# Kernel optimization log

Measured on AMD Instinct MI355X. Metric: run time of the kernel, lower is better.

## Reference

```python
import jax, jax.numpy as jnp
import numpy as np
from jax import lax

B, C, H, W = 8, 64, 64, 64
C8 = C // 8
EPS = 1e-5


def setup_inputs() -> dict:
    key = jax.random.key(0)
    ks = jax.random.split(key, 10)
    s = lambda *sh: 0.02
    inp = {
        "x": jax.random.normal(ks[0], (B, C, H, W), dtype=jnp.float32),
        "conv_b_w": jax.random.normal(ks[1], (C8, C), dtype=jnp.float32) * 0.05,
        "conv_b_b": jnp.zeros((C8,), jnp.float32),
        "conv_c_w": jax.random.normal(ks[2], (C8, C), dtype=jnp.float32) * 0.05,
        "conv_c_b": jnp.zeros((C8,), jnp.float32),
        "conv_d_w": jax.random.normal(ks[3], (C, C), dtype=jnp.float32) * 0.05,
        "conv_d_b": jnp.zeros((C,), jnp.float32),
        "alpha": jnp.zeros((1,), jnp.float32) + 0.1,  # learned PAM scale
        "beta": jnp.zeros((1,), jnp.float32) + 0.1,   # learned CAM scale
        "conv_w": jax.random.normal(ks[4], (2 * C, C, 3, 3), dtype=jnp.float32) * 0.02,
        "conv_bias": jnp.zeros((2 * C,), jnp.float32),
        "bn_gamma": jnp.ones((2 * C,), jnp.float32),
        "bn_beta": jnp.zeros((2 * C,), jnp.float32),
    }
    return inp


def _conv1x1(x, w, b):
    # x: [B,C,H,W], w: [O,C] -> [B,O,H,W]
    return jnp.einsum('oc,bchw->bohw', w, x) + b[None, :, None, None]


def _forward(x, conv_b_w, conv_b_b, conv_c_w, conv_c_b, conv_d_w, conv_d_b,
             alpha, beta, conv_w, conv_bias, bn_gamma, bn_beta):
    b, c, h, w = x.shape
    n = h * w
    # ---- Position Attention Module ----
    feat_b = _conv1x1(x, conv_b_w, conv_b_b).reshape(b, C8, n)   # [B,C8,N]
    feat_c = _conv1x1(x, conv_c_w, conv_c_b).reshape(b, C8, n)   # [B,C8,N]
    # torch: bmm(feat_b^T [B,N,C8], feat_c [B,C8,N]) -> [B,N,N]
    attn_s = jax.nn.softmax(jnp.einsum('bcn,bcm->bnm', feat_b, feat_c), axis=-1)
    feat_d = _conv1x1(x, conv_d_w, conv_d_b).reshape(b, c, n)    # [B,C,N]
    # torch: bmm(feat_d, attn_s^T) -> out[b,c,n] = sum_m feat_d[b,c,m]*attn[b,n,m]
    feat_e = jnp.einsum('bcm,bnm->bcn', feat_d, attn_s).reshape(b, c, h, w)
    x = alpha[0] * feat_e + x
    # ---- Channel Attention Module ----
    fa = x.reshape(b, c, n)                                      # [B,C,N]
    att = jnp.einsum('bcn,bdn->bcd', fa, fa)                     # [B,C,C]
    att_new = jnp.max(att, axis=-1, keepdims=True) - att
    att = jax.nn.softmax(att_new, axis=-1)
    fe = jnp.einsum('bcd,bdn->bcn', att, fa).reshape(b, c, h, w)
    x = beta[0] * fe + x
    # ---- conv3x3 + BN (batch stats) + ReLU + maxpool(2,2,pad=(1,0)) ----
    out = lax.conv_general_dilated(x, conv_w, (1, 1), ((1, 1), (1, 1)),
                                   dimension_numbers=('NCHW', 'OIHW', 'NCHW'))
    out = out + conv_bias[None, :, None, None]
    mean = jnp.mean(out, axis=(0, 2, 3), keepdims=True)
    var = jnp.var(out, axis=(0, 2, 3), keepdims=True)
    out = (out - mean) * lax.rsqrt(var + EPS)
    out = out * bn_gamma[None, :, None, None] + bn_beta[None, :, None, None]
    out = jax.nn.relu(out)
    # MaxPool2d(kernel=2, stride=2, padding=(1,0)): -inf padding on height only
    out = lax.reduce_window(out, -jnp.inf, lax.max,
                            (1, 1, 2, 2), (1, 1, 2, 2),
                            ((0, 0), (0, 0), (1, 1), (0, 0)))
    return out


def reference(x, conv_b_w, conv_b_b, conv_c_w, conv_c_b, conv_d_w, conv_d_b,
              alpha, beta, conv_w, conv_bias, bn_gamma, bn_beta):
    return _forward(x, conv_b_w, conv_b_b, conv_c_w, conv_c_b, conv_d_w, conv_d_b,
                    alpha, beta, conv_w, conv_bias, bn_gamma, bn_beta)
```

## Files before the change

### kernel.cpp

```cpp
#include <hip/hip_runtime.h>

using f32x4  = __attribute__((ext_vector_type(4))) float;
using f32x16 = __attribute__((ext_vector_type(16))) float;
using bf16x8 = __attribute__((ext_vector_type(8))) short;
using u32x4  = __attribute__((ext_vector_type(4))) unsigned int;
using u32x2  = __attribute__((ext_vector_type(2))) unsigned int;
typedef unsigned short u16;

__device__ __forceinline__ u16 f2bf(float f) {
  unsigned u = __float_as_uint(f);
  unsigned r = (u + 0x7FFFu + ((u >> 16) & 1u)) >> 16;
  return (u16)r;
}

#if __has_builtin(__builtin_amdgcn_exp2f)
#define FAST_EXP2(x) __builtin_amdgcn_exp2f(x)
#else
#define FAST_EXP2(x) __expf(0.6931471805599453f * (x))
#endif

#define LOG2E 1.4426950408889634f

__device__ __forceinline__ void permswap32(unsigned& a, unsigned& b) {
  asm volatile("v_permlane32_swap_b32 %0, %1" : "+v"(a), "+v"(b));
}

__global__ void __launch_bounds__(256) k1_conv1x1(
    const float* __restrict__ x, const float* __restrict__ wB, const float* __restrict__ bB,
    const float* __restrict__ wC, const float* __restrict__ bC,
    const float* __restrict__ wD, const float* __restrict__ bD,
    u16* __restrict__ featBb, u16* __restrict__ featCb, u16* __restrict__ featD,
    const float* __restrict__ cw, u16* __restrict__ wb) {
  const int t = threadIdx.x;
  const int b = blockIdx.y;
  const int z = blockIdx.z;
  if (z == 3) {
    int gid = (b * 16 + blockIdx.x) * 256 + t;
#pragma unroll
    for (int k = 0; k < 3; ++k) {
      int F = gid + k * 32768;
      if (F < 73728) {
        int j = F & 7, lane = (F >> 3) & 63, T = F >> 9;
        int tap = T >> 4, g = (T >> 1) & 7, kc = T & 1;
        int l16 = lane & 15, quad = lane >> 4;
        int oc = g * 16 + l16, ic = kc * 32 + quad * 8 + j;
        wb[F] = f2bf(cw[(oc * 64 + ic) * 9 + tap]);
      }
    }
    return;
  }
  __shared__ float W[2048];
  __shared__ float Bias[32];
  const int n = blockIdx.x * 256 + t;
  if (z == 0) {
    for (int i = t; i < 512; i += 256) W[i] = wB[i];
    for (int i = t; i < 512; i += 256) W[512 + i] = wC[i];
    if (t < 8) Bias[t] = bB[t];
    if (t >= 8 && t < 16) Bias[t] = bC[t - 8];
  } else {
    const float* wsrc = wD + (z - 1) * 2048;
    for (int i = t; i < 2048; i += 256) W[i] = wsrc[i];
    if (t < 32) Bias[t] = bD[(z - 1) * 32 + t];
  }
  __syncthreads();
  float xv[64];
#pragma unroll
  for (int c = 0; c < 64; ++c) xv[c] = x[((b * 64 + c) << 12) + n];
  if (z == 0) {
    float o[16];
#pragma unroll
    for (int k = 0; k < 16; ++k) {
      f32x4 s = {0.f, 0.f, 0.f, 0.f};
#pragma unroll
      for (int cq = 0; cq < 16; ++cq) {
        f32x4 wv = *(const f32x4*)&W[k * 64 + cq * 4];
        f32x4 xq = {xv[cq * 4], xv[cq * 4 + 1], xv[cq * 4 + 2], xv[cq * 4 + 3]};
        s += wv * xq;
      }
      o[k] = Bias[k] + s[0] + s[1] + s[2] + s[3];
    }
    int base = ((b << 12) + n) * 8;
    u32x4 pb, pc;
#pragma unroll
    for (int i = 0; i < 4; ++i) {
      pb[i] = (unsigned)f2bf(o[2 * i] * LOG2E) | ((unsigned)f2bf(o[2 * i + 1] * LOG2E) << 16);
      pc[i] = (unsigned)f2bf(o[8 + 2 * i]) | ((unsigned)f2bf(o[8 + 2 * i + 1]) << 16);
    }
    *(u32x4*)&featBb[base] = pb;
    *(u32x4*)&featCb[base] = pc;
  } else {
#pragma unroll 4
    for (int k = 0; k < 32; ++k) {
      f32x4 s = {0.f, 0.f, 0.f, 0.f};
#pragma unroll
      for (int cq = 0; cq < 16; ++cq) {
        f32x4 wv = *(const f32x4*)&W[k * 64 + cq * 4];
        f32x4 xq = {xv[cq * 4], xv[cq * 4 + 1], xv[cq * 4 + 2], xv[cq * 4 + 3]};
        s += wv * xq;
      }
      float val = Bias[k] + s[0] + s[1] + s[2] + s[3];
      featD[((b * 64 + (z - 1) * 32 + k) << 12) + n] = f2bf(val);
    }
  }
}

__global__ void __launch_bounds__(256) k2_pam_part(
    const u16* __restrict__ fBb, const u16* __restrict__ fCb, const u16* __restrict__ fD,
    u16* __restrict__ numPart, float* __restrict__ denPart) {
  __shared__ u16 Df[64 * 132];
  const int t = threadIdx.x, b = blockIdx.y, z = blockIdx.z;
  const int w = t >> 6, lane = t & 63, l32 = lane & 31, hi = lane >> 5;
  const int nb = blockIdx.x * 128 + w * 32;
  const int mz = z << 10;

  bf16x8 bq = (bf16x8)(short)0;
  if (hi == 0) bq = *(const bf16x8*)&fBb[(((b << 12) + nb + l32) << 3)];

  f32x16 acc[2];
#pragma unroll
  for (int ct = 0; ct < 2; ++ct) acc[ct] = (f32x16)(0.0f);
  float denp = 0.f;

  for (int ch = 0; ch < 8; ++ch) {
    const int m0 = mz + (ch << 7);
    __syncthreads();
#pragma unroll
    for (int hh = 0; hh < 4; ++hh) {
      int idx = hh * 256 + t;
      int r = idx >> 4, mo = (idx & 15) << 3;
      *(u32x4*)&Df[r * 132 + mo] = *(const u32x4*)&fD[((b * 64 + r) << 12) + m0 + mo];
    }
    __syncthreads();
#pragma unroll
    for (int mt2 = 0; mt2 < 4; ++mt2) {
      bf16x8 af = (bf16x8)(short)0;
      if (hi == 0) af = *(const bf16x8*)&fCb[(((b << 12) + m0 + mt2 * 32 + l32) << 3)];

      unsigned u0[8];
      {
        f32x16 s = __builtin_amdgcn_mfma_f32_32x32x16_bf16(af, bq, (f32x16)(0.0f), 0, 0, 0);
        float dsum = 0.f;
#pragma unroll
        for (int i = 0; i < 8; ++i) {
          float e0 = FAST_EXP2(s[2 * i]);
          float e1 = FAST_EXP2(s[2 * i + 1]);
          dsum += e0 + e1;
          u0[i] = __builtin_amdgcn_perm(__float_as_uint(e1), __float_as_uint(e0), 0x07060302u);
        }
        denp += dsum;
      }
      permswap32(u0[0], u0[2]); permswap32(u0[1], u0[3]);
      permswap32(u0[4], u0[6]); permswap32(u0[5], u0[7]);

#pragma unroll
      for (int kc = 0; kc < 2; ++kc) {
        u32x4 q0 = {u0[4 * kc], u0[4 * kc + 1], u0[4 * kc + 2], u0[4 * kc + 3]};
        bf16x8 bv0 = *(bf16x8*)&q0;
#pragma unroll
        for (int ct = 0; ct < 2; ++ct) {
          bf16x8 av = *(const bf16x8*)&Df[(ct * 32 + l32) * 132 + mt2 * 32 + kc * 16 + hi * 8];
          acc[ct] = __builtin_amdgcn_mfma_f32_32x32x16_bf16(av, bv0, acc[ct], 0, 0, 0);
        }
      }
    }
  }

  const int zb = z * 8 + b;
#pragma unroll
  for (int ct = 0; ct < 2; ++ct)
#pragma unroll
    for (int r = 0; r < 16; ++r) {
      int c = ct * 32 + (r & 3) + ((r >> 2) << 3) + (hi << 2);
      numPart[((zb * 64 + c) << 12) + nb + l32] = (u16)(__float_as_uint(acc[ct][r]) >> 16);
    }
  {
    float d = denp + __shfl_xor(denp, 32);
    if (hi == 0) denPart[(zb << 12) + nb + l32] = d;
  }
}

__global__ void __launch_bounds__(256) k3_gram(
    const u16* __restrict__ numPart, const float* __restrict__ denPart,
    const float* __restrict__ x, const float* __restrict__ alpha,
    float* __restrict__ x1, float* __restrict__ attPart) {
  __shared__ float X[64 * 132];
  __shared__ float Dinv[128];
  const int t = threadIdx.x, b = blockIdx.y, cx = blockIdx.x;
  const int n0 = cx * 128;
  if (t < 128) {
    float den = 0.f;
#pragma unroll
    for (int z = 0; z < 4; ++z) den += denPart[(((z * 8 + b) << 12)) + n0 + t];
    Dinv[t] = alpha[0] / den;
  }
  __syncthreads();
  for (int idx = t; idx < 4096; idx += 256) {
    int row = idx >> 6, cp = (idx & 63) * 2;
    int gi = ((b * 64 + row) << 12) + n0 + cp;
    float num0 = 0.f, num1 = 0.f;
#pragma unroll
    for (int z = 0; z < 4; ++z) {
      unsigned v = *(const unsigned*)&numPart[(((z * 8 + b) * 64 + row) << 12) + n0 + cp];
      num0 += __uint_as_float(v << 16);
      num1 += __uint_as_float(v & 0xFFFF0000u);
    }
    float v0 = num0 * Dinv[cp] + x[gi];
    float v1 = num1 * Dinv[cp + 1] + x[gi + 1];
    X[row * 132 + cp] = v0;
    X[row * 132 + cp + 1] = v1;
    x1[gi] = v0;
    x1[gi + 1] = v1;
  }
  __syncthreads();
  const int cg = t >> 4, dg = t & 15;
  f32x4 acc[4][4];
#pragma unroll
  for (int i = 0; i < 4; ++i)
#pragma unroll
    for (int k = 0; k < 4; ++k) acc[i][k] = (f32x4){0.f, 0.f, 0.f, 0.f};
  for (int nq0 = 0; nq0 < 32; ++nq0) {
    int nq = (nq0 + dg) & 31;
    f32x4 a[4], bb[4];
#pragma unroll
    for (int i = 0; i < 4; ++i) a[i] = *(const f32x4*)&X[(cg * 4 + i) * 132 + nq * 4];
#pragma unroll
    for (int k = 0; k < 4; ++k) bb[k] = *(const f32x4*)&X[(dg * 4 + k) * 132 + nq * 4];
#pragma unroll
    for (int i = 0; i < 4; ++i)
#pragma unroll
      for (int k = 0; k < 4; ++k) acc[i][k] += a[i] * bb[k];
  }
#pragma unroll
  for (int i = 0; i < 4; ++i)
#pragma unroll
    for (int k = 0; k < 4; ++k) {
      f32x4 s = acc[i][k];
      attPart[((b * 32 + cx) * 64 + cg * 4 + i) * 64 + dg * 4 + k] = s[0] + s[1] + s[2] + s[3];
    }
}

__global__ void __launch_bounds__(256) k4_softmax(const float* __restrict__ attPart, float* __restrict__ attP) {
  const int b = blockIdx.y, t = threadIdx.x;
  const int c = (blockIdx.x << 2) + (t >> 6), d = t & 63;
  float v = 0.f;
  for (int p = 0; p < 32; ++p) v += attPart[((b * 32 + p) * 64 + c) * 64 + d];
  float mn = v;
#pragma unroll
  for (int off = 1; off < 64; off <<= 1) mn = fminf(mn, __shfl_xor(mn, off));
  float e = __expf(mn - v);
  float sum = e;
#pragma unroll
  for (int off = 1; off < 64; off <<= 1) sum += __shfl_xor(sum, off);
  attP[(b * 64 + c) * 64 + d] = e / sum;
}

__global__ void __launch_bounds__(256) k5_apply(
    const float* __restrict__ attP, const float* __restrict__ x1,
    const float* __restrict__ beta, u16* __restrict__ x2b) {
  __shared__ float A[64 * 68];
  const int t = threadIdx.x, b = blockIdx.y;
  for (int idx = t; idx < 4096; idx += 256) A[(idx >> 6) * 68 + (idx & 63)] = attP[(b << 12) + idx];
  __syncthreads();
  const int n = blockIdx.x * 64 + (t & 63);
  const int cq = t >> 6;
  const float bv = beta[0];
  float acc[16];
#pragma unroll
  for (int i = 0; i < 16; ++i) acc[i] = 0.f;
  const float* xcol = x1 + ((size_t)b << 18) + n;
#pragma unroll 4
  for (int dq = 0; dq < 16; ++dq) {
    float x0 = xcol[(size_t)(dq * 4 + 0) << 12];
    float x1v = xcol[(size_t)(dq * 4 + 1) << 12];
    float x2 = xcol[(size_t)(dq * 4 + 2) << 12];
    float x3 = xcol[(size_t)(dq * 4 + 3) << 12];
#pragma unroll
    for (int i = 0; i < 16; ++i) {
      const float* av = &A[(cq * 16 + i) * 68 + dq * 4];
      acc[i] += av[0] * x0 + av[1] * x1v + av[2] * x2 + av[3] * x3;
    }
  }
  u16* orow = x2b + ((((size_t)(b << 12) + n) << 6) + cq * 16);
  unsigned pk[8];
#pragma unroll
  for (int i = 0; i < 16; i += 2) {
    float v0 = bv * acc[i] + xcol[(size_t)(cq * 16 + i) << 12];
    float v1 = bv * acc[i + 1] + xcol[(size_t)(cq * 16 + i + 1) << 12];
    pk[i >> 1] = (unsigned)f2bf(v0) | ((unsigned)f2bf(v1) << 16);
  }
  *(u32x4*)&orow[0] = *(u32x4*)&pk[0];
  *(u32x4*)&orow[8] = *(u32x4*)&pk[4];
}

__global__ void __launch_bounds__(256) k6_mfma(const u16* __restrict__ x2b, const u16* __restrict__ wb,
                                               float* __restrict__ y) {
  __shared__ u16 Xl[3 * 66 * 72];
  const int t = threadIdx.x, b = blockIdx.y, h = blockIdx.x;
  for (int idx = t; idx < 3 * 66 * 8; idx += 256) {
    int r = idx / 528;
    int rem = idx - r * 528;
    int c = rem >> 3, icq = rem & 7;
    int gy = h - 1 + r, gx = c - 1;
    u32x4 v = {0u, 0u, 0u, 0u};
    if (gy >= 0 && gy < 64 && gx >= 0 && gx < 64)
      v = *(const u32x4*)&x2b[(((size_t)(b << 6 | gy) << 6) + gx) * 64 + icq * 8];
    *(u32x4*)&Xl[(r * 66 + c) * 72 + icq * 8] = v;
  }
  __syncthreads();
  const int w = t >> 6, lane = t & 63, quad = lane >> 4, l16 = lane & 15;
  const int mBase = (w & 1) * 64;
  const int og = (w & 1) * 4;
  const int nBase = (w >> 1) * 32;
  f32x4 acc[4][2];
#pragma unroll
  for (int ot = 0; ot < 4; ++ot)
#pragma unroll
    for (int nt = 0; nt < 2; ++nt) acc[ot][nt] = (f32x4){0.f, 0.f, 0.f, 0.f};
#pragma unroll 3
  for (int tap = 0; tap < 9; ++tap) {
    const int dy = tap / 3, dx = tap - dy * 3;
    bf16x8 af[4][2];
#pragma unroll
    for (int ot = 0; ot < 4; ++ot)
#pragma unroll
      for (int kc = 0; kc < 2; ++kc)
        af[ot][kc] = *(const bf16x8*)&wb[((((tap * 8 + og + ot) * 2 + kc) << 6) + lane) << 3];
#pragma unroll
    for (int nt = 0; nt < 2; ++nt) {
      const int prow = dy * 66 + nBase + nt * 16 + l16 + dx;
#pragma unroll
      for (int kc = 0; kc < 2; ++kc) {
        bf16x8 bv = *(const bf16x8*)&Xl[prow * 72 + kc * 32 + quad * 8];
#pragma unroll
        for (int ot = 0; ot < 4; ++ot)
          acc[ot][nt] = __builtin_amdgcn_mfma_f32_16x16x32_bf16(af[ot][kc], bv, acc[ot][nt], 0, 0, 0);
      }
    }
  }
#pragma unroll
  for (int ot = 0; ot < 4; ++ot)
#pragma unroll
    for (int nt = 0; nt < 2; ++nt)
#pragma unroll
      for (int r = 0; r < 4; ++r) {
        int oc = mBase + ot * 16 + quad * 4 + r;
        int pix = nBase + nt * 16 + l16;
        y[((b * 128 + oc) << 12) + (h << 6) + pix] = acc[ot][nt][r];
      }
}

__global__ void __launch_bounds__(256) k7_part(const float* __restrict__ y, float* __restrict__ pstats) {
  const int ch = blockIdx.x, q = blockIdx.y, t = threadIdx.x;
  float s = 0.f, ss = 0.f;
#pragma unroll
  for (int bb = 0; bb < 2; ++bb) {
    const float* p = y + (((q * 2 + bb) * 128 + ch) << 12);
#pragma unroll
    for (int i = 0; i < 16; ++i) { float v = p[i * 256 + t]; s += v; ss += v * v; }
  }
#pragma unroll
  for (int off = 1; off < 64; off <<= 1) { s += __shfl_xor(s, off); ss += __shfl_xor(ss, off); }
  __shared__ float rs[4], rss[4];
  if ((t & 63) == 0) { rs[t >> 6] = s; rss[t >> 6] = ss; }
  __syncthreads();
  if (t == 0) {
    pstats[ch * 8 + q * 2]     = rs[0] + rs[1] + rs[2] + rs[3];
    pstats[ch * 8 + q * 2 + 1] = rss[0] + rss[1] + rss[2] + rss[3];
  }
}

__global__ void __launch_bounds__(256) k8_pool(const float* __restrict__ y, const float* __restrict__ pstats,
                                               const float* __restrict__ gamma, const float* __restrict__ bbeta,
                                               float* __restrict__ out) {
  const int bc = blockIdx.x;
  const int ch = bc & 127;
  float S = 0.f, SS = 0.f;
#pragma unroll
  for (int q = 0; q < 4; ++q) { S += pstats[ch * 8 + q * 2]; SS += pstats[ch * 8 + q * 2 + 1]; }
  const float mean = S * (1.f / 32768.f);
  const float var = SS * (1.f / 32768.f) - mean * mean;
  const float sc = gamma[ch] * rsqrtf(var + 1e-5f);
  const float sh = bbeta[ch] - mean * sc;
  const float* p = y + (bc << 12);
  float* op = out + bc * (33 * 32);
  for (int i = threadIdx.x; i < 33 * 32; i += 256) {
    int oh = i >> 5, ow = i & 31;
    int r0 = 2 * oh - 1, r1 = 2 * oh;
    float m = 0.f;
    if (r0 >= 0) {
      m = fmaxf(m, p[r0 * 64 + 2 * ow] * sc + sh);
      m = fmaxf(m, p[r0 * 64 + 2 * ow + 1] * sc + sh);
    }
    if (r1 <= 63) {
      m = fmaxf(m, p[r1 * 64 + 2 * ow] * sc + sh);
      m = fmaxf(m, p[r1 * 64 + 2 * ow + 1] * sc + sh);
    }
    op[i] = m;
  }
}

extern "C" void kernel_launch(void* const* d_in, const int* in_sizes, int n_in,
                              void* d_out, int out_size, void* d_ws, size_t ws_size,
                              hipStream_t stream) {
  const float* x      = (const float*)d_in[0];
  const float* wB     = (const float*)d_in[1];
  const float* bB     = (const float*)d_in[2];
  const float* wC     = (const float*)d_in[3];
  const float* bC     = (const float*)d_in[4];
  const float* wD     = (const float*)d_in[5];
  const float* bD     = (const float*)d_in[6];
  const float* alpha  = (const float*)d_in[7];
  const float* beta   = (const float*)d_in[8];
  const float* cw     = (const float*)d_in[9];
  const float* gamma  = (const float*)d_in[11];
  const float* bnbeta = (const float*)d_in[12];

  char* ws = (char*)d_ws;
  u16*   featBb  = (u16*)  (ws + 0);
  u16*   featCb  = (u16*)  (ws + 524288);
  u16*   fDb     = (u16*)  (ws + 1048576);
  u16*   x2b     = (u16*)  (ws + 0);
  float* x1      = (float*)(ws + 5242880);
  u16*   numPart = (u16*)  (ws + 13631488);
  float* y       = (float*)(ws + 13631488);
  float* denPart = (float*)(ws + 30408704);
  float* attPart = (float*)(ws + 30932992);
  float* attP    = (float*)(ws + 35127296);
  u16*   wb      = (u16*)  (ws + 35258368);
  float* pstats  = (float*)(ws + 35405824);
  float* outp    = (float*)d_out;

  k1_conv1x1<<<dim3(16, 8, 4), 256, 0, stream>>>(x, wB, bB, wC, bC, wD, bD, featBb, featCb, fDb, cw, wb);
  k2_pam_part<<<dim3(32, 8, 4), 256, 0, stream>>>(featBb, featCb, fDb, numPart, denPart);
  k3_gram<<<dim3(32, 8), 256, 0, stream>>>(numPart, denPart, x, alpha, x1, attPart);
  k4_softmax<<<dim3(16, 8), 256, 0, stream>>>(attPart, attP);
  k5_apply<<<dim3(64, 8), 256, 0, stream>>>(attP, x1, beta, x2b);
  k6_mfma<<<dim3(64, 8), 256, 0, stream>>>(x2b, wb, y);
  k7_part<<<dim3(128, 4), 256, 0, stream>>>(y, pstats);
  k8_pool<<<dim3(1024), 256, 0, stream>>>(y, pstats, gamma, bnbeta, outp);
}
```

Measured before the change: 190.9 us.

## Double-buffer PAM value tiles and compute softmax denominator with MFMA

The k2_pam_part kernel now prefetches the next 128-column chunk of feat_d into registers while the current chunk is processed. It stores that chunk into a second LDS buffer, so each iteration needs one barrier instead of two. The four fCb query fragments are loaded up front, ahead of the MFMAs. The softmax denominator is now a third MFMA against a ones-row A operand instead of VALU adds and a cross-lane shuffle. This adds an MFMA per step and more LDS and registers, in exchange for less VALU work and less exposed global-load latency.

```diff
diff --git a/kernel.cpp b/kernel.cpp
--- a/kernel.cpp
+++ b/kernel.cpp
@@ -107,47 +107,66 @@
 __global__ void __launch_bounds__(256) k2_pam_part(
     const u16* __restrict__ fBb, const u16* __restrict__ fCb, const u16* __restrict__ fD,
     u16* __restrict__ numPart, float* __restrict__ denPart) {
-  __shared__ u16 Df[64 * 132];
+  __shared__ u16 Df[2][64 * 132];
   const int t = threadIdx.x, b = blockIdx.y, z = blockIdx.z;
   const int w = t >> 6, lane = t & 63, l32 = lane & 31, hi = lane >> 5;
   const int nb = blockIdx.x * 128 + w * 32;
   const int mz = z << 10;
 
+  int srow[4], smo[4];
+#pragma unroll
+  for (int hh = 0; hh < 4; ++hh) {
+    int idx = hh * 256 + t;
+    srow[hh] = idx >> 4;
+    smo[hh] = (idx & 15) << 3;
+  }
+
   bf16x8 bq = (bf16x8)(short)0;
   if (hi == 0) bq = *(const bf16x8*)&fBb[(((b << 12) + nb + l32) << 3)];
 
-  f32x16 acc[2];
-#pragma unroll
-  for (int ct = 0; ct < 2; ++ct) acc[ct] = (f32x16)(0.0f);
-  float denp = 0.f;
-
+  bf16x8 onesA = (bf16x8)(short)0;
+  if (l32 == 0) onesA = (bf16x8)(short)0x3F80;
+
+  f32x16 acc0 = (f32x16)(0.0f), acc1 = (f32x16)(0.0f), accd = (f32x16)(0.0f);
+
+  u32x4 sreg[4];
+#define K2_ISSUE(CH) {                                                        \
+    int m0_ = mz + ((CH) << 7);                                               \
+    _Pragma("unroll")                                                         \
+    for (int hh = 0; hh < 4; ++hh)                                            \
+      sreg[hh] = *(const u32x4*)&fD[((b * 64 + srow[hh]) << 12) + m0_ + smo[hh]]; }
+#define K2_WRITE(BUF) {                                                       \
+    _Pragma("unroll")                                                         \
+    for (int hh = 0; hh < 4; ++hh)                                            \
+      *(u32x4*)&Df[BUF][srow[hh] * 132 + smo[hh]] = sreg[hh]; }
+
+  K2_ISSUE(0);
+  K2_WRITE(0);
+  __syncthreads();
+
+#pragma unroll 2
   for (int ch = 0; ch < 8; ++ch) {
+    const int cur = ch & 1;
     const int m0 = mz + (ch << 7);
-    __syncthreads();
-#pragma unroll
-    for (int hh = 0; hh < 4; ++hh) {
-      int idx = hh * 256 + t;
-      int r = idx >> 4, mo = (idx & 15) << 3;
-      *(u32x4*)&Df[r * 132 + mo] = *(const u32x4*)&fD[((b * 64 + r) << 12) + m0 + mo];
-    }
-    __syncthreads();
+    if (ch < 7) K2_ISSUE(ch + 1);
+
+    bf16x8 afv[4];
 #pragma unroll
     for (int mt2 = 0; mt2 < 4; ++mt2) {
-      bf16x8 af = (bf16x8)(short)0;
-      if (hi == 0) af = *(const bf16x8*)&fCb[(((b << 12) + m0 + mt2 * 32 + l32) << 3)];
-
+      bf16x8 a = (bf16x8)(short)0;
+      if (hi == 0) a = *(const bf16x8*)&fCb[(((b << 12) + m0 + mt2 * 32 + l32) << 3)];
+      afv[mt2] = a;
+    }
+
+#pragma unroll
+    for (int mt2 = 0; mt2 < 4; ++mt2) {
+      f32x16 s = __builtin_amdgcn_mfma_f32_32x32x16_bf16(afv[mt2], bq, (f32x16)(0.0f), 0, 0, 0);
       unsigned u0[8];
-      {
-        f32x16 s = __builtin_amdgcn_mfma_f32_32x32x16_bf16(af, bq, (f32x16)(0.0f), 0, 0, 0);
-        float dsum = 0.f;
-#pragma unroll
-        for (int i = 0; i < 8; ++i) {
-          float e0 = FAST_EXP2(s[2 * i]);
-          float e1 = FAST_EXP2(s[2 * i + 1]);
-          dsum += e0 + e1;
-          u0[i] = __builtin_amdgcn_perm(__float_as_uint(e1), __float_as_uint(e0), 0x07060302u);
-        }
-        denp += dsum;
+#pragma unroll
+      for (int i = 0; i < 8; ++i) {
+        float e0 = FAST_EXP2(s[2 * i]);
+        float e1 = FAST_EXP2(s[2 * i + 1]);
+        u0[i] = __builtin_amdgcn_perm(__float_as_uint(e1), __float_as_uint(e0), 0x07060302u);
       }
       permswap32(u0[0], u0[2]); permswap32(u0[1], u0[3]);
       permswap32(u0[4], u0[6]); permswap32(u0[5], u0[7]);
@@ -156,27 +175,28 @@
       for (int kc = 0; kc < 2; ++kc) {
         u32x4 q0 = {u0[4 * kc], u0[4 * kc + 1], u0[4 * kc + 2], u0[4 * kc + 3]};
         bf16x8 bv0 = *(bf16x8*)&q0;
-#pragma unroll
-        for (int ct = 0; ct < 2; ++ct) {
-          bf16x8 av = *(const bf16x8*)&Df[(ct * 32 + l32) * 132 + mt2 * 32 + kc * 16 + hi * 8];
-          acc[ct] = __builtin_amdgcn_mfma_f32_32x32x16_bf16(av, bv0, acc[ct], 0, 0, 0);
-        }
-      }
-    }
-  }
+        bf16x8 av0 = *(const bf16x8*)&Df[cur][(l32) * 132 + mt2 * 32 + kc * 16 + hi * 8];
+        bf16x8 av1 = *(const bf16x8*)&Df[cur][(32 + l32) * 132 + mt2 * 32 + kc * 16 + hi * 8];
+        acc0 = __builtin_amdgcn_mfma_f32_32x32x16_bf16(av0, bv0, acc0, 0, 0, 0);
+        acc1 = __builtin_amdgcn_mfma_f32_32x32x16_bf16(av1, bv0, acc1, 0, 0, 0);
+        accd = __builtin_amdgcn_mfma_f32_32x32x16_bf16(onesA, bv0, accd, 0, 0, 0);
+      }
+    }
+
+    if (ch < 7) K2_WRITE(cur ^ 1);
+    __syncthreads();
+  }
+#undef K2_ISSUE
+#undef K2_WRITE
 
   const int zb = z * 8 + b;
 #pragma unroll
-  for (int ct = 0; ct < 2; ++ct)
-#pragma unroll
-    for (int r = 0; r < 16; ++r) {
-      int c = ct * 32 + (r & 3) + ((r >> 2) << 3) + (hi << 2);
-      numPart[((zb * 64 + c) << 12) + nb + l32] = (u16)(__float_as_uint(acc[ct][r]) >> 16);
-    }
-  {
-    float d = denp + __shfl_xor(denp, 32);
-    if (hi == 0) denPart[(zb << 12) + nb + l32] = d;
-  }
+  for (int r = 0; r < 16; ++r) {
+    int c = (r & 3) + ((r >> 2) << 3) + (hi << 2);
+    numPart[((zb * 64 + c) << 12) + nb + l32] = (u16)(__float_as_uint(acc0[r]) >> 16);
+    numPart[((zb * 64 + c + 32) << 12) + nb + l32] = (u16)(__float_as_uint(acc1[r]) >> 16);
+  }
+  if (hi == 0) denPart[(zb << 12) + nb + l32] = accd[0];
 }
 
 __global__ void __launch_bounds__(256) k3_gram(
```

Measured after the change: 184.0 us. 1.04x faster.
